# Kernel optimization log

Hardware: AMD Instinct MI355X
Metric: run time of the kernel (lower is better)

The kernel has to match this reference:

```python
import jax, jax.numpy as jnp
import numpy as np

L = 104          # atom feature / hidden dim (self.length)
NUM_CLASSES = 500
D, N, P = 256, 1024, 8  # DAGs, nodes per DAG (topo-ordered), max predecessors


def setup_inputs() -> dict:
    key = jax.random.key(0)
    ks = jax.random.split(key, 8)
    atom_features = jax.random.normal(ks[0], (D, N, L), dtype=jnp.float32)

    # Padded predecessor lists; pred_idx[d, n, p] < n guarantees topological order 0..N-1.
    rng = np.random.default_rng(0)
    base = np.floor(rng.random((D, N, P)) * np.maximum(np.arange(N), 1)[None, :, None]).astype(np.int32)
    keep = rng.random((D, N, P)) < 0.6
    keep[:, :, 0] = True                      # every non-root node has >=1 predecessor
    pred_idx = np.where(keep, base, -1)
    pred_idx[:, 0, :] = -1                    # node 0 is the root (no predecessors)
    pred_idx = jnp.asarray(pred_idx, dtype=jnp.int32)

    s1 = float(1.0 / np.sqrt(L))
    s2 = float(1.0 / np.sqrt(2 * L))
    W_single = jax.random.uniform(ks[1], (L, L), minval=-s1, maxval=s1)
    b_single = jax.random.uniform(ks[2], (L,), minval=-s1, maxval=s1)
    W_merge = jax.random.uniform(ks[3], (L, 2 * L), minval=-s2, maxval=s2)
    b_merge = jax.random.uniform(ks[4], (L,), minval=-s2, maxval=s2)
    attn_w = jax.random.uniform(ks[5], (L,))   # torch.rand(length)
    dag_w = jax.random.uniform(ks[6], (L,))
    W_final = jax.random.uniform(ks[7], (NUM_CLASSES, L), minval=-s1, maxval=s1)
    b_final = jnp.zeros((NUM_CLASSES,), jnp.float32)
    return {
        "atom_features": atom_features, "pred_idx": pred_idx,
        "W_single": W_single, "b_single": b_single,
        "W_merge": W_merge, "b_merge": b_merge,
        "attn_w": attn_w, "dag_w": dag_w,
        "W_final": W_final, "b_final": b_final,
    }


def _forward(atom_features, pred_idx, W_single, b_single, W_merge, b_merge,
             attn_w, dag_w, W_final, b_final):
    n_nodes = atom_features.shape[1]

    def per_dag(feats, preds):  # feats [N, L], preds [N, P]
        def step(outputs, n):
            feat = feats[n]                                   # [L]
            p = preds[n]                                      # [P]
            valid = p >= 0                                    # [P]
            po = outputs[jnp.clip(p, 0, n_nodes - 1)]         # [P, L] gathered predecessor outputs
            # softmax over the predecessor (stacking) dim, weighted by attention_weight
            logits = jnp.where(valid[:, None], attn_w * po, -1e30)
            agg = jnp.sum(jax.nn.softmax(logits, axis=0) * po * valid[:, None].astype(po.dtype), axis=0)  # [L]
            merged = jax.nn.relu(W_merge @ jnp.concatenate([agg, feat]) + b_merge)
            root = jax.nn.relu(W_single @ feat + b_single)
            out = jnp.where(jnp.any(valid), merged, root)     # [L]
            return outputs.at[n].set(out), None
        outputs, _ = jax.lax.scan(step, jnp.zeros_like(feats), jnp.arange(n_nodes))
        return outputs[-1]                                    # output of last (sink) node

    last = jax.vmap(per_dag)(atom_features, pred_idx)         # [D, L]
    w = jax.nn.softmax(dag_w * last, axis=0)                  # softmax over DAG dim
    pooled = jnp.sum(w * last, axis=0)                        # [L]
    return pooled @ W_final.T + b_final                       # [NUM_CLASSES]


def reference(atom_features, pred_idx, W_single, b_single, W_merge, b_merge,
              attn_w, dag_w, W_final, b_final):
    return _forward(atom_features, pred_idx, W_single, b_single, W_merge, b_merge,
                    attn_w, dag_w, W_final, b_final)
```

## Files before the change

### kernel.cpp

```cpp
#include <hip/hip_runtime.h>

#define DN  256
#define NN  1024
#define PP  8
#define LL  104
#define CLS 500
#define BT  512
#define TMAX 64
#define KP  232
#define NG  26

typedef __attribute__((ext_vector_type(8))) short short8;
typedef __attribute__((ext_vector_type(4))) short short4v;
typedef __attribute__((ext_vector_type(4))) float f32x4;

#define MFMA(a, b, c) __builtin_amdgcn_mfma_f32_16x16x32_bf16((a), (b), (c), 0, 0, 0)

__device__ __forceinline__ void split_bf16(float x, unsigned short& h, unsigned short& l) {
    unsigned u = __float_as_uint(x);
    h = (unsigned short)(u >> 16);
    float hf = __uint_as_float(u & 0xFFFF0000u);
    l = (unsigned short)(__float_as_uint(x - hf) >> 16);
}

__device__ __forceinline__ void sm_store(int ni, int lg, const int pi[PP],
    const float4 pv[PP], float4 ft, const float* s_attn2,
    unsigned short (*xh)[KP], unsigned short (*xl)[KP])
{
    float4 aw = *(const float4*)&s_attn2[lg * 4];
    float awv[4] = {aw.x, aw.y, aw.z, aw.w};
    float ftv[4] = {ft.x, ft.y, ft.z, ft.w};
    unsigned short oh[8], ol[8];
    #pragma unroll
    for (int f = 0; f < 4; ++f) {
        float den = 0.f, num = 0.f;
        #pragma unroll
        for (int q = 0; q < PP; ++q) {
            float pvq = ((const float*)&pv[q])[f];
            float e2 = exp2f(awv[f] * pvq);
            e2 = (pi[q] >= 0) ? e2 : 0.f;
            den += e2;
            num = fmaf(e2, pvq, num);
        }
        float agg = __fdividef(num, den);
        split_bf16(agg,    oh[f],     ol[f]);
        split_bf16(ftv[f], oh[4 + f], ol[4 + f]);
    }
    short4v h0 = {(short)oh[0], (short)oh[1], (short)oh[2], (short)oh[3]};
    short4v l0 = {(short)ol[0], (short)ol[1], (short)ol[2], (short)ol[3]};
    short4v h1 = {(short)oh[4], (short)oh[5], (short)oh[6], (short)oh[7]};
    short4v l1 = {(short)ol[4], (short)ol[5], (short)ol[6], (short)ol[7]};
    *(short4v*)&xh[ni][lg*4]      = h0;
    *(short4v*)&xl[ni][lg*4]      = l0;
    *(short4v*)&xh[ni][LL + lg*4] = h1;
    *(short4v*)&xl[ni][LL + lg*4] = l1;
}

__global__ __launch_bounds__(BT, 2) void dag_level_kernel(
    const float* __restrict__ atom,
    const int*   __restrict__ pred,
    const float* __restrict__ W_single,
    const float* __restrict__ b_single,
    const float* __restrict__ W_merge,
    const float* __restrict__ b_merge,
    const float* __restrict__ attn_w,
    float* __restrict__ out_all,
    float* __restrict__ last_buf)
{
    __shared__ __align__(16) unsigned short x_hi[TMAX][KP];
    __shared__ __align__(16) unsigned short x_lo[TMAX][KP];
    __shared__ __align__(16) int pred_lds[NN][PP];
    __shared__ __align__(16) float out_lds[TMAX][LL];
    __shared__ int   lvl[NN];
    __shared__ int   cnt[NN];
    __shared__ unsigned short order[NN];
    __shared__ unsigned short pos_lds[NN];
    __shared__ __align__(16) float s_attn2[LL];
    __shared__ float s_bm[LL];
    __shared__ int   csum[64];
    __shared__ int   s_flag, s_maxlvl;

    const int d    = blockIdx.x;
    const int tid  = threadIdx.x;
    const int wid  = tid >> 6;
    const int lane = tid & 63;

    const float* atom_d = atom + (size_t)d * NN * LL;
    const int*   pred_d = pred + (size_t)d * NN * PP;
    float*       out_d  = out_all + (size_t)d * NN * LL;

    for (int idx = tid; idx < NN * PP / 4; idx += BT)
        ((int4*)pred_lds)[idx] = ((const int4*)pred_d)[idx];

    short8 wh[7], wl[7];
    {
        const int r = min(wid, 6)*16 + (lane & 15);
        #pragma unroll
        for (int kt = 0; kt < 7; ++kt) {
            const int k0 = kt*32 + (lane >> 4)*8;
            short8 hh, lo8;
            #pragma unroll
            for (int j = 0; j < 8; ++j) {
                float v = (r < LL && (k0 + j) < 2*LL) ? W_merge[r*2*LL + k0 + j] : 0.f;
                unsigned short a, b;
                split_bf16(v, a, b);
                hh[j] = (short)a; lo8[j] = (short)b;
            }
            wh[kt] = hh; wl[kt] = lo8;
        }
    }

    for (int idx = tid; idx < TMAX * (KP - 2*LL); idx += BT) {
        int rr = idx / (KP - 2*LL), cc = 2*LL + (idx - rr*(KP - 2*LL));
        x_hi[rr][cc] = 0; x_lo[rr][cc] = 0;
    }
    if (tid < LL) { s_attn2[tid] = attn_w[tid] * 1.44269504f; s_bm[tid] = b_merge[tid]; }
    if (tid == 0) { s_flag = 0; s_maxlvl = 0; }
    lvl[tid] = 0; lvl[tid + BT] = 0;
    __syncthreads();

    {
        int mypA[PP], mypB[PP];
        #pragma unroll
        for (int q = 0; q < PP; ++q) { mypA[q] = pred_lds[tid][q]; mypB[q] = pred_lds[tid + BT][q]; }
        for (int it = 1; it <= NN; ++it) {
            bool ch = false;
            #pragma unroll
            for (int rep = 0; rep < 2; ++rep) {
                int mxA = -1, mxB = -1;
                #pragma unroll
                for (int q = 0; q < PP; ++q) {
                    if (mypA[q] >= 0) mxA = max(mxA, lvl[mypA[q]]);
                    if (mypB[q] >= 0) mxB = max(mxB, lvl[mypB[q]]);
                }
                if (mxA + 1 != lvl[tid])      { lvl[tid]      = mxA + 1; ch = true; }
                if (mxB + 1 != lvl[tid + BT]) { lvl[tid + BT] = mxB + 1; ch = true; }
            }
            if (ch) s_flag = it;
            __syncthreads();
            int f = s_flag;
            __syncthreads();
            if (f != it) break;
        }
        atomicMax(&s_maxlvl, max(lvl[tid], lvl[tid + BT]));
    }

    cnt[tid] = 0; cnt[tid + BT] = 0;
    __syncthreads();
    atomicAdd(&cnt[lvl[tid]], 1);
    atomicAdd(&cnt[lvl[tid + BT]], 1);
    __syncthreads();
    if (tid < 64) { int s = 0; for (int i = 0; i < 16; ++i) s += cnt[tid*16 + i]; csum[tid] = s; }
    __syncthreads();
    if (tid == 0) { int run = 0; for (int t = 0; t < 64; ++t) { int c = csum[t]; csum[t] = run; run += c; } }
    __syncthreads();
    if (tid < 64) {
        int run = csum[tid];
        for (int i = 0; i < 16; ++i) { int c = cnt[tid*16 + i]; cnt[tid*16 + i] = run; run += c; }
    }
    __syncthreads();
    {
        int pos = atomicAdd(&cnt[lvl[tid]], 1);
        order[pos] = (unsigned short)tid;      pos_lds[tid] = (unsigned short)pos;
        pos = atomicAdd(&cnt[lvl[tid + BT]], 1);
        order[pos] = (unsigned short)(tid + BT); pos_lds[tid + BT] = (unsigned short)pos;
    }
    __syncthreads();

    {
        int nroots = cnt[0];
        for (int task = tid; task < nroots * LL; task += BT) {
            int ni = task / LL, r = task - ni * LL;
            int n = order[ni];
            float acc = b_single[r];
            const float* feat = atom_d + n * LL;
            const float* wr = W_single + r * LL;
            #pragma unroll 8
            for (int l = 0; l < LL; ++l) acc = fmaf(wr[l], feat[l], acc);
            float v = fmaxf(acc, 0.f);
            out_d[n * LL + r] = v;
            if (ni < TMAX) out_lds[ni][r] = v;
            if (n == NN - 1) last_buf[d * LL + r] = v;
        }
    }
    __syncthreads();

    const int maxlvl = s_maxlvl;

    float4 pf_po[PP];
    float4 pf_ft = {0.f, 0.f, 0.f, 0.f};
    int    pf_fresh = 0;

#define PREFETCH(NT0, NTC, CT0, CTC) do {                                      \
        pf_fresh = 0;                                                          \
        if (tid < (NTC) * NG) {                                                \
            int ni_ = tid / NG, lg_ = tid - ni_ * NG;                          \
            int n_ = order[(NT0) + ni_];                                       \
            pf_ft = *(const float4*)&atom_d[n_ * LL + lg_ * 4];                \
            _Pragma("unroll")                                                  \
            for (int q_ = 0; q_ < PP; ++q_) {                                  \
                int pi_ = pred_lds[n_][q_];                                    \
                unsigned rel_ = (unsigned)((int)pos_lds[max(pi_, 0)] - (CT0)); \
                bool il_ = (pi_ >= 0) && (rel_ < (unsigned)(CTC));             \
                pf_fresh |= (il_ ? 1 : 0) << q_;                               \
                int row_ = il_ ? 0 : max(pi_, 0);                              \
                pf_po[q_] = *(const float4*)&out_d[row_ * LL + lg_ * 4];       \
            }                                                                  \
        }                                                                      \
    } while (0)

    int pt0 = 0, ptc = cnt[0];

    if (maxlvl >= 1) {
        int s1 = cnt[0];
        PREFETCH(s1, min(TMAX, cnt[1] - s1), 0, ptc);
    }

    for (int L = 1; L <= maxlvl; ++L) {
        const int s = cnt[L - 1], e = cnt[L];
        for (int t0 = s; t0 < e; t0 += TMAX) {
            const int tc = min(TMAX, e - t0);
            const int ntask = tc * NG;

            if (tid < ntask) {
                int ni = tid / NG, lg = tid - ni * NG;
                int n = order[t0 + ni];
                int pi[PP];
                #pragma unroll
                for (int q = 0; q < PP; ++q) pi[q] = pred_lds[n][q];
                float4 pv[PP];
                #pragma unroll
                for (int q = 0; q < PP; ++q) {
                    bool il = (pf_fresh >> q) & 1;
                    int slot = il ? ((int)pos_lds[max(pi[q], 0)] - pt0) : 0;
                    float4 lv = *(const float4*)&out_lds[slot][lg * 4];
                    pv[q] = il ? lv : pf_po[q];
                }
                sm_store(ni, lg, pi, pv, pf_ft, s_attn2, x_hi, x_lo);
            }
            for (int task = tid + BT; task < ntask; task += BT) {
                int ni = task / NG, lg = task - ni * NG;
                int n = order[t0 + ni];
                int pi[PP]; int ilm = 0; int slot[PP];
                #pragma unroll
                for (int q = 0; q < PP; ++q) {
                    pi[q] = pred_lds[n][q];
                    int rel = (int)pos_lds[max(pi[q], 0)] - pt0;
                    bool il = (pi[q] >= 0) && ((unsigned)rel < (unsigned)ptc);
                    ilm |= (il ? 1 : 0) << q;
                    slot[q] = il ? rel : 0;
                }
                float4 gv[PP];
                #pragma unroll
                for (int q = 0; q < PP; ++q) {
                    int row = ((ilm >> q) & 1) ? 0 : max(pi[q], 0);
                    gv[q] = *(const float4*)&out_d[row * LL + lg * 4];
                }
                float4 pv[PP];
                #pragma unroll
                for (int q = 0; q < PP; ++q) {
                    float4 lv = *(const float4*)&out_lds[slot[q]][lg * 4];
                    pv[q] = ((ilm >> q) & 1) ? lv : gv[q];
                }
                float4 ft = *(const float4*)&atom_d[n * LL + lg * 4];
                sm_store(ni, lg, pi, pv, ft, s_attn2, x_hi, x_lo);
            }
            __syncthreads();

            {
                int nt0 = 0, ntc = 0;
                if (t0 + TMAX < e)        { nt0 = t0 + TMAX; ntc = min(TMAX, e - nt0); }
                else if (L + 1 <= maxlvl) { nt0 = e;         ntc = min(TMAX, cnt[L + 1] - e); }
                PREFETCH(nt0, ntc, t0, tc);
            }

            if (wid < 7) {
                const int mts = (tc + 15) >> 4;
                const int kg = (lane >> 4) * 8;
                const int r0 = wid*16 + (lane & 15);
                for (int mt = 0; mt < mts; ++mt) {
                    const int row_a = mt*16 + (lane & 15);
                    f32x4 a0 = {0.f,0.f,0.f,0.f}, b0 = {0.f,0.f,0.f,0.f}, c0 = {0.f,0.f,0.f,0.f};
                    #pragma unroll
                    for (int kt = 0; kt < 7; ++kt) {
                        const int k0 = kt*32 + kg;
                        short8 ah = *(const short8*)&x_hi[row_a][k0];
                        short8 al = *(const short8*)&x_lo[row_a][k0];
                        a0 = MFMA(ah, wh[kt], a0);
                        b0 = MFMA(ah, wl[kt], b0);
                        c0 = MFMA(al, wh[kt], c0);
                    }
                    f32x4 acc = a0 + b0 + c0;
                    if (r0 < LL) {
                        #pragma unroll
                        for (int j = 0; j < 4; ++j) {
                            int ni = mt*16 + (lane >> 4)*4 + j;
                            if (ni < tc) {
                                int n = order[t0 + ni];
                                float v = fmaxf(acc[j] + s_bm[r0], 0.f);
                                out_d[n*LL + r0] = v;
                                out_lds[ni][r0] = v;
                                if (n == NN - 1) last_buf[d*LL + r0] = v;
                            }
                        }
                    }
                }
            }
            __syncthreads();
            pt0 = t0; ptc = tc;
        }
    }
#undef PREFETCH
}

__global__ __launch_bounds__(256) void final_pool_kernel(
    const float* __restrict__ last_buf,
    const float* __restrict__ dag_w,
    const float* __restrict__ W_final,
    const float* __restrict__ b_final,
    float* __restrict__ out)
{
    __shared__ float s_pooled[LL];
    const int tid = threadIdx.x;

    if (tid < LL) {
        float dw = dag_w[tid];
        float m = -1e30f;
        #pragma unroll 8
        for (int dd = 0; dd < DN; ++dd)
            m = fmaxf(m, dw * last_buf[dd * LL + tid]);
        float den = 0.f, num = 0.f;
        #pragma unroll 8
        for (int dd = 0; dd < DN; ++dd) {
            float v = last_buf[dd * LL + tid];
            float e = __expf(dw * v - m);
            den += e;
            num = fmaf(e, v, num);
        }
        s_pooled[tid] = num / den;
    }
    __syncthreads();

    for (int c = tid; c < CLS; c += 256) {
        float acc = b_final[c];
        const float* wr = W_final + c * LL;
        #pragma unroll 8
        for (int l = 0; l < LL; ++l) acc = fmaf(wr[l], s_pooled[l], acc);
        out[c] = acc;
    }
}

extern "C" void kernel_launch(void* const* d_in, const int* in_sizes, int n_in,
                              void* d_out, int out_size, void* d_ws, size_t ws_size,
                              hipStream_t stream) {
    const float* atom     = (const float*)d_in[0];
    const int*   pred     = (const int*)  d_in[1];
    const float* W_single = (const float*)d_in[2];
    const float* b_single = (const float*)d_in[3];
    const float* W_merge  = (const float*)d_in[4];
    const float* b_merge  = (const float*)d_in[5];
    const float* attn_w   = (const float*)d_in[6];
    const float* dag_w    = (const float*)d_in[7];
    const float* W_final  = (const float*)d_in[8];
    const float* b_final  = (const float*)d_in[9];
    float* out = (float*)d_out;

    float* out_all  = (float*)d_ws;
    float* last_buf = out_all + (size_t)DN * NN * LL;

    dag_level_kernel<<<DN, BT, 0, stream>>>(atom, pred, W_single, b_single,
                                            W_merge, b_merge, attn_w,
                                            out_all, last_buf);
    final_pool_kernel<<<1, 256, 0, stream>>>(last_buf, dag_w, W_final, b_final, out);
}
```

Baseline: 373.6 us.

## Precompute predecessor positions, defer global output stores, pre-split features to bf16

Replaces the per-node predecessor table in LDS with a table of each predecessor's position in level order. This removes the indirection through pos_lds on every gather and lets freshness be tested with a single compare. The MFMA epilogue now writes results only to LDS. The copy of each tile's outputs to global memory is deferred and overlapped with the next tile's gather phase, using threads that are idle or finished. Feature bf16 hi/lo splitting moves into the prefetch, which shortens the softmax store path. The cost is more complex ordering invariants, and the final tile's rows are never flushed to out_all.

```diff
diff --git a/kernel.cpp b/kernel.cpp
--- a/kernel.cpp
+++ b/kernel.cpp
@@ -23,14 +23,13 @@
     l = (unsigned short)(__float_as_uint(x - hf) >> 16);
 }
 
-__device__ __forceinline__ void sm_store(int ni, int lg, const int pi[PP],
-    const float4 pv[PP], float4 ft, const float* s_attn2,
+__device__ __forceinline__ void sm_store2(int ni, int lg, int vmask,
+    const float4 pv[PP], short4v fth, short4v ftl, const float* s_attn2,
     unsigned short (*xh)[KP], unsigned short (*xl)[KP])
 {
     float4 aw = *(const float4*)&s_attn2[lg * 4];
     float awv[4] = {aw.x, aw.y, aw.z, aw.w};
-    float ftv[4] = {ft.x, ft.y, ft.z, ft.w};
-    unsigned short oh[8], ol[8];
+    unsigned short oh[4], ol[4];
     #pragma unroll
     for (int f = 0; f < 4; ++f) {
         float den = 0.f, num = 0.f;
@@ -38,22 +37,17 @@
         for (int q = 0; q < PP; ++q) {
             float pvq = ((const float*)&pv[q])[f];
             float e2 = exp2f(awv[f] * pvq);
-            e2 = (pi[q] >= 0) ? e2 : 0.f;
+            e2 = ((vmask >> q) & 1) ? e2 : 0.f;
             den += e2;
             num = fmaf(e2, pvq, num);
         }
         float agg = __fdividef(num, den);
-        split_bf16(agg,    oh[f],     ol[f]);
-        split_bf16(ftv[f], oh[4 + f], ol[4 + f]);
-    }
-    short4v h0 = {(short)oh[0], (short)oh[1], (short)oh[2], (short)oh[3]};
-    short4v l0 = {(short)ol[0], (short)ol[1], (short)ol[2], (short)ol[3]};
-    short4v h1 = {(short)oh[4], (short)oh[5], (short)oh[6], (short)oh[7]};
-    short4v l1 = {(short)ol[4], (short)ol[5], (short)ol[6], (short)ol[7]};
-    *(short4v*)&xh[ni][lg*4]      = h0;
-    *(short4v*)&xl[ni][lg*4]      = l0;
-    *(short4v*)&xh[ni][LL + lg*4] = h1;
-    *(short4v*)&xl[ni][LL + lg*4] = l1;
+        split_bf16(agg, oh[f], ol[f]);
+    }
+    *(short4v*)&xh[ni][lg*4] = (short4v){(short)oh[0], (short)oh[1], (short)oh[2], (short)oh[3]};
+    *(short4v*)&xl[ni][lg*4] = (short4v){(short)ol[0], (short)ol[1], (short)ol[2], (short)ol[3]};
+    *(short4v*)&xh[ni][LL + lg*4] = fth;
+    *(short4v*)&xl[ni][LL + lg*4] = ftl;
 }
 
 __global__ __launch_bounds__(BT, 2) void dag_level_kernel(
@@ -69,7 +63,7 @@
 {
     __shared__ __align__(16) unsigned short x_hi[TMAX][KP];
     __shared__ __align__(16) unsigned short x_lo[TMAX][KP];
-    __shared__ __align__(16) int pred_lds[NN][PP];
+    __shared__ __align__(16) unsigned short ppos_lds[NN][PP];
     __shared__ __align__(16) float out_lds[TMAX][LL];
     __shared__ int   lvl[NN];
     __shared__ int   cnt[NN];
@@ -88,9 +82,6 @@
     const float* atom_d = atom + (size_t)d * NN * LL;
     const int*   pred_d = pred + (size_t)d * NN * PP;
     float*       out_d  = out_all + (size_t)d * NN * LL;
-
-    for (int idx = tid; idx < NN * PP / 4; idx += BT)
-        ((int4*)pred_lds)[idx] = ((const int4*)pred_d)[idx];
 
     short8 wh[7], wl[7];
     {
@@ -117,33 +108,40 @@
     if (tid < LL) { s_attn2[tid] = attn_w[tid] * 1.44269504f; s_bm[tid] = b_merge[tid]; }
     if (tid == 0) { s_flag = 0; s_maxlvl = 0; }
     lvl[tid] = 0; lvl[tid + BT] = 0;
-    __syncthreads();
-
+
+    int mypA[PP], mypB[PP];
     {
-        int mypA[PP], mypB[PP];
+        const int4* p4 = (const int4*)(pred_d + tid * PP);
+        int4 a = p4[0], b = p4[1];
+        mypA[0]=a.x; mypA[1]=a.y; mypA[2]=a.z; mypA[3]=a.w;
+        mypA[4]=b.x; mypA[5]=b.y; mypA[6]=b.z; mypA[7]=b.w;
+        const int4* q4 = (const int4*)(pred_d + (tid + BT) * PP);
+        int4 c = q4[0], e = q4[1];
+        mypB[0]=c.x; mypB[1]=c.y; mypB[2]=c.z; mypB[3]=c.w;
+        mypB[4]=e.x; mypB[5]=e.y; mypB[6]=e.z; mypB[7]=e.w;
+    }
+    __syncthreads();
+
+    for (int it = 1; it <= NN; ++it) {
+        bool ch = false;
         #pragma unroll
-        for (int q = 0; q < PP; ++q) { mypA[q] = pred_lds[tid][q]; mypB[q] = pred_lds[tid + BT][q]; }
-        for (int it = 1; it <= NN; ++it) {
-            bool ch = false;
+        for (int rep = 0; rep < 2; ++rep) {
+            int mxA = -1, mxB = -1;
             #pragma unroll
-            for (int rep = 0; rep < 2; ++rep) {
-                int mxA = -1, mxB = -1;
-                #pragma unroll
-                for (int q = 0; q < PP; ++q) {
-                    if (mypA[q] >= 0) mxA = max(mxA, lvl[mypA[q]]);
-                    if (mypB[q] >= 0) mxB = max(mxB, lvl[mypB[q]]);
-                }
-                if (mxA + 1 != lvl[tid])      { lvl[tid]      = mxA + 1; ch = true; }
-                if (mxB + 1 != lvl[tid + BT]) { lvl[tid + BT] = mxB + 1; ch = true; }
-            }
-            if (ch) s_flag = it;
-            __syncthreads();
-            int f = s_flag;
-            __syncthreads();
-            if (f != it) break;
-        }
-        atomicMax(&s_maxlvl, max(lvl[tid], lvl[tid + BT]));
-    }
+            for (int q = 0; q < PP; ++q) {
+                if (mypA[q] >= 0) mxA = max(mxA, lvl[mypA[q]]);
+                if (mypB[q] >= 0) mxB = max(mxB, lvl[mypB[q]]);
+            }
+            if (mxA + 1 != lvl[tid])      { lvl[tid]      = mxA + 1; ch = true; }
+            if (mxB + 1 != lvl[tid + BT]) { lvl[tid + BT] = mxB + 1; ch = true; }
+        }
+        if (ch) s_flag = it;
+        __syncthreads();
+        int f = s_flag;
+        __syncthreads();
+        if (f != it) break;
+    }
+    atomicMax(&s_maxlvl, max(lvl[tid], lvl[tid + BT]));
 
     cnt[tid] = 0; cnt[tid + BT] = 0;
     __syncthreads();
@@ -161,12 +159,27 @@
     __syncthreads();
     {
         int pos = atomicAdd(&cnt[lvl[tid]], 1);
-        order[pos] = (unsigned short)tid;      pos_lds[tid] = (unsigned short)pos;
+        order[pos] = (unsigned short)tid;        pos_lds[tid] = (unsigned short)pos;
         pos = atomicAdd(&cnt[lvl[tid + BT]], 1);
         order[pos] = (unsigned short)(tid + BT); pos_lds[tid + BT] = (unsigned short)pos;
     }
     __syncthreads();
 
+    {
+        unsigned short tA[PP], tB[PP];
+        #pragma unroll
+        for (int q = 0; q < PP; ++q) {
+            tA[q] = (mypA[q] < 0) ? (unsigned short)0xFFFFu : pos_lds[mypA[q]];
+            tB[q] = (mypB[q] < 0) ? (unsigned short)0xFFFFu : pos_lds[mypB[q]];
+        }
+        int pA = pos_lds[tid], pB = pos_lds[tid + BT];
+        *(short4v*)&ppos_lds[pA][0] = (short4v){(short)tA[0],(short)tA[1],(short)tA[2],(short)tA[3]};
+        *(short4v*)&ppos_lds[pA][4] = (short4v){(short)tA[4],(short)tA[5],(short)tA[6],(short)tA[7]};
+        *(short4v*)&ppos_lds[pB][0] = (short4v){(short)tB[0],(short)tB[1],(short)tB[2],(short)tB[3]};
+        *(short4v*)&ppos_lds[pB][4] = (short4v){(short)tB[4],(short)tB[5],(short)tB[6],(short)tB[7]};
+    }
+
+    __syncthreads();
     {
         int nroots = cnt[0];
         for (int task = tid; task < nroots * LL; task += BT) {
@@ -187,23 +200,25 @@
 
     const int maxlvl = s_maxlvl;
 
-    float4 pf_po[PP];
-    float4 pf_ft = {0.f, 0.f, 0.f, 0.f};
-    int    pf_fresh = 0;
-
-#define PREFETCH(NT0, NTC, CT0, CTC) do {                                      \
-        pf_fresh = 0;                                                          \
+    float4  pf_po[PP];
+    short4v pf_fth = {0,0,0,0}, pf_ftl = {0,0,0,0};
+
+#define PREFETCH(NT0, NTC, CT0) do {                                           \
         if (tid < (NTC) * NG) {                                                \
             int ni_ = tid / NG, lg_ = tid - ni_ * NG;                          \
             int n_ = order[(NT0) + ni_];                                       \
-            pf_ft = *(const float4*)&atom_d[n_ * LL + lg_ * 4];                \
+            float4 ft_ = *(const float4*)&atom_d[n_ * LL + lg_ * 4];           \
+            unsigned short h0_,h1_,h2_,h3_,l0_,l1_,l2_,l3_;                    \
+            split_bf16(ft_.x, h0_, l0_); split_bf16(ft_.y, h1_, l1_);          \
+            split_bf16(ft_.z, h2_, l2_); split_bf16(ft_.w, h3_, l3_);          \
+            pf_fth = (short4v){(short)h0_,(short)h1_,(short)h2_,(short)h3_};   \
+            pf_ftl = (short4v){(short)l0_,(short)l1_,(short)l2_,(short)l3_};   \
+            short8 pps_ = *(const short8*)&ppos_lds[(NT0) + ni_][0];           \
             _Pragma("unroll")                                                  \
             for (int q_ = 0; q_ < PP; ++q_) {                                  \
-                int pi_ = pred_lds[n_][q_];                                    \
-                unsigned rel_ = (unsigned)((int)pos_lds[max(pi_, 0)] - (CT0)); \
-                bool il_ = (pi_ >= 0) && (rel_ < (unsigned)(CTC));             \
-                pf_fresh |= (il_ ? 1 : 0) << q_;                               \
-                int row_ = il_ ? 0 : max(pi_, 0);                              \
+                int pp_ = (unsigned short)pps_[q_];                            \
+                bool old_ = (pp_ != 0xFFFF) && (pp_ < (CT0));                  \
+                int row_ = old_ ? (int)order[pp_] : 0;                         \
                 pf_po[q_] = *(const float4*)&out_d[row_ * LL + lg_ * 4];       \
             }                                                                  \
         }                                                                      \
@@ -213,7 +228,7 @@
 
     if (maxlvl >= 1) {
         int s1 = cnt[0];
-        PREFETCH(s1, min(TMAX, cnt[1] - s1), 0, ptc);
+        PREFETCH(s1, min(TMAX, cnt[1] - s1), 0);
     }
 
     for (int L = 1; L <= maxlvl; ++L) {
@@ -221,49 +236,66 @@
         for (int t0 = s; t0 < e; t0 += TMAX) {
             const int tc = min(TMAX, e - t0);
             const int ntask = tc * NG;
-
-            if (tid < ntask) {
+            const int pcopy = ptc * NG;
+            const bool has_task = tid < ntask;
+
+            if (!has_task) {
+                for (int ct = (BT - 1) - tid; ct < pcopy; ct += BT) {
+                    int ci = ct / NG, lg = ct - ci * NG;
+                    int n = order[pt0 + ci];
+                    *(float4*)&out_d[n * LL + lg * 4] = *(const float4*)&out_lds[ci][lg * 4];
+                }
+            }
+            if (has_task) {
                 int ni = tid / NG, lg = tid - ni * NG;
-                int n = order[t0 + ni];
-                int pi[PP];
+                short8 pps = *(const short8*)&ppos_lds[t0 + ni][0];
+                float4 pv[PP]; int vmask = 0;
                 #pragma unroll
-                for (int q = 0; q < PP; ++q) pi[q] = pred_lds[n][q];
+                for (int q = 0; q < PP; ++q) {
+                    int pp = (unsigned short)pps[q];
+                    bool valid = pp != 0xFFFF;
+                    bool fresh = valid && pp >= pt0;
+                    vmask |= (valid ? 1 : 0) << q;
+                    int slot = fresh ? (pp - pt0) : 0;
+                    float4 lv = *(const float4*)&out_lds[slot][lg * 4];
+                    pv[q] = fresh ? lv : pf_po[q];
+                }
+                sm_store2(ni, lg, vmask, pv, pf_fth, pf_ftl, s_attn2, x_hi, x_lo);
+                for (int ct = (BT - 1) - tid; ct < pcopy; ct += BT) {
+                    int ci = ct / NG, lg2 = ct - ci * NG;
+                    int n = order[pt0 + ci];
+                    *(float4*)&out_d[n * LL + lg2 * 4] = *(const float4*)&out_lds[ci][lg2 * 4];
+                }
+            }
+            for (int task = tid + BT; task < ntask; task += BT) {
+                int ni = task / NG, lg = task - ni * NG;
+                short8 pps = *(const short8*)&ppos_lds[t0 + ni][0];
+                int vmask = 0; int slotv[PP]; float4 gv[PP];
+                #pragma unroll
+                for (int q = 0; q < PP; ++q) {
+                    int pp = (unsigned short)pps[q];
+                    bool valid = pp != 0xFFFF;
+                    bool fresh = valid && pp >= pt0;
+                    vmask |= (valid ? 1 : 0) << q;
+                    slotv[q] = fresh ? (pp - pt0) : -1;
+                    int row = (valid && !fresh) ? (int)order[pp] : 0;
+                    gv[q] = *(const float4*)&out_d[row * LL + lg * 4];
+                }
                 float4 pv[PP];
                 #pragma unroll
                 for (int q = 0; q < PP; ++q) {
-                    bool il = (pf_fresh >> q) & 1;
-                    int slot = il ? ((int)pos_lds[max(pi[q], 0)] - pt0) : 0;
-                    float4 lv = *(const float4*)&out_lds[slot][lg * 4];
-                    pv[q] = il ? lv : pf_po[q];
-                }
-                sm_store(ni, lg, pi, pv, pf_ft, s_attn2, x_hi, x_lo);
-            }
-            for (int task = tid + BT; task < ntask; task += BT) {
-                int ni = task / NG, lg = task - ni * NG;
+                    int sl = slotv[q] >= 0 ? slotv[q] : 0;
+                    float4 lv = *(const float4*)&out_lds[sl][lg * 4];
+                    pv[q] = (slotv[q] >= 0) ? lv : gv[q];
+                }
                 int n = order[t0 + ni];
-                int pi[PP]; int ilm = 0; int slot[PP];
-                #pragma unroll
-                for (int q = 0; q < PP; ++q) {
-                    pi[q] = pred_lds[n][q];
-                    int rel = (int)pos_lds[max(pi[q], 0)] - pt0;
-                    bool il = (pi[q] >= 0) && ((unsigned)rel < (unsigned)ptc);
-                    ilm |= (il ? 1 : 0) << q;
-                    slot[q] = il ? rel : 0;
-                }
-                float4 gv[PP];
-                #pragma unroll
-                for (int q = 0; q < PP; ++q) {
-                    int row = ((ilm >> q) & 1) ? 0 : max(pi[q], 0);
-                    gv[q] = *(const float4*)&out_d[row * LL + lg * 4];
-                }
-                float4 pv[PP];
-                #pragma unroll
-                for (int q = 0; q < PP; ++q) {
-                    float4 lv = *(const float4*)&out_lds[slot[q]][lg * 4];
-                    pv[q] = ((ilm >> q) & 1) ? lv : gv[q];
-                }
                 float4 ft = *(const float4*)&atom_d[n * LL + lg * 4];
-                sm_store(ni, lg, pi, pv, ft, s_attn2, x_hi, x_lo);
+                unsigned short h0,h1,h2,h3,l0,l1,l2,l3;
+                split_bf16(ft.x, h0, l0); split_bf16(ft.y, h1, l1);
+                split_bf16(ft.z, h2, l2); split_bf16(ft.w, h3, l3);
+                short4v fth = (short4v){(short)h0,(short)h1,(short)h2,(short)h3};
+                short4v ftl = (short4v){(short)l0,(short)l1,(short)l2,(short)l3};
+                sm_store2(ni, lg, vmask, pv, fth, ftl, s_attn2, x_hi, x_lo);
             }
             __syncthreads();
 
@@ -271,7 +303,7 @@
                 int nt0 = 0, ntc = 0;
                 if (t0 + TMAX < e)        { nt0 = t0 + TMAX; ntc = min(TMAX, e - nt0); }
                 else if (L + 1 <= maxlvl) { nt0 = e;         ntc = min(TMAX, cnt[L + 1] - e); }
-                PREFETCH(nt0, ntc, t0, tc);
+                PREFETCH(nt0, ntc, t0);
             }
 
             if (wid < 7) {
@@ -296,10 +328,9 @@
                         for (int j = 0; j < 4; ++j) {
                             int ni = mt*16 + (lane >> 4)*4 + j;
                             if (ni < tc) {
+                                float v = fmaxf(acc[j] + s_bm[r0], 0.f);
+                                out_lds[ni][r0] = v;
                                 int n = order[t0 + ni];
-                                float v = fmaxf(acc[j] + s_bm[r0], 0.f);
-                                out_d[n*LL + r0] = v;
-                                out_lds[ni][r0] = v;
                                 if (n == NN - 1) last_buf[d*LL + r0] = v;
                             }
                         }
```

After: 378.3 us. Within noise of the previous version (+1.2%).
